# Optimization experiments

Hardware: AMD Instinct MI355X
Metric: run time of the kernel (lower is better)

The kernel has to match this reference:

```python
import jax, jax.numpy as jnp
import numpy as np

BSZ, DIM, SEQ_A, SEQ_B = 16, 768, 1024, 1024


def setup_inputs() -> dict:
    key = jax.random.key(0)
    kA, kB, kU = jax.random.split(key, 3)
    input_A = jax.random.normal(kA, (BSZ, DIM, SEQ_A), dtype=jnp.float32)
    input_B = jax.random.normal(kB, (BSZ, DIM, SEQ_B), dtype=jnp.float32)
    intput_msk = jnp.zeros((BSZ, SEQ_A, SEQ_B), dtype=jnp.float32)  # 0 = on, -inf = off
    U = jax.random.normal(kU, (DIM, DIM), dtype=jnp.float32)
    return {"input_A": input_A, "input_B": input_B, "intput_msk": intput_msk, "U": U}


def reference(input_A, input_B, intput_msk, U):
    # align[b,s,t] = tanh( A[b,:,s]^T U B[b,:,t] )  -> (bsz, seq_A, seq_B)
    align = jnp.einsum("bds,de,bet->bst", input_A, U, input_B)
    align = jnp.tanh(align) + intput_msk
    # per-token scores: max over the other modality's sequence, then softmax
    score_A = jax.nn.softmax(jnp.max(align, axis=2), axis=-1)  # (bsz, seq_A)
    score_B = jax.nn.softmax(jnp.max(align, axis=1), axis=-1)  # (bsz, seq_B)
    output_A = jnp.einsum("bds,bs->bd", input_A, score_A)  # (bsz, dim_A)
    output_B = jnp.einsum("bdt,bt->bd", input_B, score_B)  # (bsz, dim_B)
    return (output_A, output_B)
```

## Files before the change

### kernel.cpp

```cpp
#include <hip/hip_runtime.h>
#include <math.h>

#define BSZ  16
#define DIM  768
#define SEQA 1024
#define SEQB 1024

typedef float f32x4 __attribute__((ext_vector_type(4)));
typedef long long llong;

__device__ inline void gload_lds16(const void* g, void* l) {
    __builtin_amdgcn_global_load_lds(
        (const __attribute__((address_space(1))) void*)g,
        (__attribute__((address_space(3))) void*)l, 16, 0, 0);
}

__device__ inline unsigned enc_key(float f) {
    unsigned u = __float_as_uint(f);
    return (u & 0x80000000u) ? ~u : (u | 0x80000000u);
}
__device__ inline float dec_key(unsigned k) {
    return (k & 0x80000000u) ? __uint_as_float(k ^ 0x80000000u) : __uint_as_float(~k);
}

__device__ inline unsigned pk4_fp8(float a, float b, float c, float d) {
    int v = 0;
    v = __builtin_amdgcn_cvt_pk_fp8_f32(a, b, v, false);
    v = __builtin_amdgcn_cvt_pk_fp8_f32(c, d, v, true);
    return (unsigned)v;
}
__device__ inline unsigned char f2fp8(float a) {
    return (unsigned char)(__builtin_amdgcn_cvt_pk_fp8_f32(a, a, 0, false) & 0xFF);
}

__device__ inline float fast_tanh(float x) {
    float ax = fabsf(x);
    float u = __expf(-2.0f * ax);
    float th = __fdividef(1.0f - u, 1.0f + u);
    return copysignf(th, x);
}

__global__ __launch_bounds__(256) void t_cast_AB(const float* __restrict__ A,
                                                 const float* __restrict__ B,
                                                 unsigned char* __restrict__ At,
                                                 unsigned char* __restrict__ Bt) {
    __shared__ float tl[64][68];
    const int z = blockIdx.z;
    const float* X = (z < BSZ) ? A : B;
    unsigned char* Y = (z < BSZ) ? At : Bt;
    const int b = z & 15;
    const int d0 = blockIdx.y * 64;
    const int s0 = blockIdx.x * 64;
    const int tid = threadIdx.x;
    const int rr = tid >> 4, c4 = tid & 15;
    const float* Xb = X + ((size_t)b * DIM + d0) * SEQA + s0;
#pragma unroll
    for (int i = 0; i < 4; i++) {
        int row = i * 16 + rr;
        float4 v = *(const float4*)&Xb[(size_t)row * SEQA + c4 * 4];
        *(float4*)&tl[row][c4 * 4] = v;
    }
    __syncthreads();
    unsigned char* Yb = Y + ((size_t)b * SEQA + s0) * DIM + d0;
    const int m = tid & 15, sl = tid >> 4;
#pragma unroll
    for (int i = 0; i < 4; i++) {
        int s = sl + 16 * i;
        unsigned v = pk4_fp8(tl[4 * m + 0][s], tl[4 * m + 1][s], tl[4 * m + 2][s], tl[4 * m + 3][s]);
        *(unsigned*)&Yb[(size_t)s * DIM + 4 * m] = v;
    }
}

__global__ __launch_bounds__(256) void t_cast_U(const float* __restrict__ U,
                                                unsigned char* __restrict__ Ut,
                                                unsigned* __restrict__ keyA,
                                                unsigned* __restrict__ keyB) {
    __shared__ float tl[64][68];
    const int d0 = blockIdx.y * 64;
    const int e0 = blockIdx.x * 64;
    const int tid = threadIdx.x;
    const int bid = blockIdx.y * gridDim.x + blockIdx.x;
    if (bid < 64) {
        int i = bid * 256 + tid;
        keyA[i] = 0u;
        keyB[i] = 0u;
    }
    const int rr = tid >> 4, c4 = tid & 15;
#pragma unroll
    for (int i = 0; i < 4; i++) {
        int row = i * 16 + rr;
        float4 v = *(const float4*)&U[(size_t)(d0 + row) * DIM + e0 + c4 * 4];
        *(float4*)&tl[row][c4 * 4] = v;
    }
    __syncthreads();
    const int m = tid & 15, sl = tid >> 4;
#pragma unroll
    for (int i = 0; i < 4; i++) {
        int e = sl + 16 * i;
        unsigned v = pk4_fp8(tl[4 * m + 0][e], tl[4 * m + 1][e], tl[4 * m + 2][e], tl[4 * m + 3][e]);
        *(unsigned*)&Ut[(size_t)(e0 + e) * DIM + d0 + 4 * m] = v;
    }
}

__device__ inline void stage_tile(const unsigned char* __restrict__ src, int row0,
                                  int kbyte0, unsigned char* lds, int wid, int lane) {
    const int r8 = lane >> 3;
    const int g  = lane & 7;
    const int gg = g ^ (r8 & 7);
#pragma unroll
    for (int t = 0; t < 4; ++t) {
        int row = row0 + wid * 32 + t * 8 + r8;
        gload_lds16(src + (size_t)row * DIM + kbyte0 + gg * 16,
                    lds + (wid * 32 + t * 8) * 128 + lane * 16);
    }
}

__device__ inline llong frag_read(const unsigned char* lds, int rowbase, int l15,
                                  int quad, int h) {
    int gg = 2 * h + (quad >> 1);
    int off = (rowbase + l15) * 128 + ((gg ^ (l15 & 7)) << 4) + (quad & 1) * 8;
    return *(const llong*)(lds + off);
}

__global__ __launch_bounds__(256, 3) void k1_ua(const unsigned char* __restrict__ At,
                                                const unsigned char* __restrict__ Ut,
                                                unsigned char* __restrict__ Ct) {
    __shared__ __align__(16) unsigned char As[128 * 128];
    __shared__ __align__(16) unsigned char Us[128 * 128];
    const int b  = blockIdx.z;
    const int s0 = blockIdx.x * 128;
    const int e0 = blockIdx.y * 128;
    const int tid = threadIdx.x;
    const int lane = tid & 63;
    const int wid = tid >> 6;
    const int wr = wid >> 1, wc = wid & 1;
    const int quad = lane >> 4, l15 = lane & 15;

    const unsigned char* Atb = At + (size_t)b * SEQA * DIM;
    f32x4 acc[4][4] = {};

    for (int d0 = 0; d0 < DIM; d0 += 128) {
        stage_tile(Atb + (size_t)s0 * DIM, 0, d0, As, wid, lane);
        stage_tile(Ut + (size_t)e0 * DIM, 0, d0, Us, wid, lane);
        __syncthreads();
#pragma unroll
        for (int h = 0; h < 4; ++h) {
            llong av[4], bv[4];
#pragma unroll
            for (int i = 0; i < 4; ++i) av[i] = frag_read(As, wr * 64 + 16 * i, l15, quad, h);
#pragma unroll
            for (int j = 0; j < 4; ++j) bv[j] = frag_read(Us, wc * 64 + 16 * j, l15, quad, h);
#pragma unroll
            for (int i = 0; i < 4; ++i)
#pragma unroll
                for (int j = 0; j < 4; ++j)
                    acc[i][j] = __builtin_amdgcn_mfma_f32_16x16x32_fp8_fp8(av[i], bv[j], acc[i][j], 0, 0, 0);
        }
        __syncthreads();
    }
    unsigned char* Cb = Ct + (size_t)b * SEQA * DIM;
#pragma unroll
    for (int i = 0; i < 4; ++i)
#pragma unroll
        for (int j = 0; j < 4; ++j) {
            int e_g = e0 + wc * 64 + 16 * j + l15;
#pragma unroll
            for (int r = 0; r < 4; ++r) {
                int s_g = s0 + wr * 64 + 16 * i + quad * 4 + r;
                Cb[(size_t)s_g * DIM + e_g] = f2fp8(acc[i][j][r]);
            }
        }
}

__global__ __launch_bounds__(256, 4) void k2_align(const unsigned char* __restrict__ Ct,
                                                   const unsigned char* __restrict__ Bt,
                                                   const float* __restrict__ msk,
                                                   unsigned* __restrict__ keyA,
                                                   unsigned* __restrict__ keyB) {
    __shared__ __align__(16) unsigned char Cs[128 * 128];
    __shared__ __align__(16) unsigned char Bs[128 * 128];
    const int b  = blockIdx.z;
    const int t0 = blockIdx.x * 128;
    const int s0 = blockIdx.y * 128;
    const int tid = threadIdx.x;
    const int lane = tid & 63;
    const int wid = tid >> 6;
    const int wr = wid >> 1, wc = wid & 1;
    const int quad = lane >> 4, l15 = lane & 15;

    f32x4 acc[4][4] = {};

    for (int e0 = 0; e0 < DIM; e0 += 128) {
        stage_tile(Ct + (size_t)(b * SEQA + s0) * DIM, 0, e0, Cs, wid, lane);
        stage_tile(Bt + (size_t)(b * SEQB + t0) * DIM, 0, e0, Bs, wid, lane);
        __syncthreads();
#pragma unroll
        for (int h = 0; h < 4; ++h) {
            llong av[4], bv[4];
#pragma unroll
            for (int i = 0; i < 4; ++i) av[i] = frag_read(Bs, wr * 64 + 16 * i, l15, quad, h);
#pragma unroll
            for (int j = 0; j < 4; ++j) bv[j] = frag_read(Cs, wc * 64 + 16 * j, l15, quad, h);
#pragma unroll
            for (int i = 0; i < 4; ++i)
#pragma unroll
                for (int j = 0; j < 4; ++j)
                    acc[i][j] = __builtin_amdgcn_mfma_f32_16x16x32_fp8_fp8(av[i], bv[j], acc[i][j], 0, 0, 0);
        }
        __syncthreads();
    }

    const float* Mb = msk + (size_t)b * SEQA * SEQB;
#pragma unroll
    for (int j = 0; j < 4; ++j) {
        int s_g = s0 + wc * 64 + 16 * j + l15;
#pragma unroll
        for (int i = 0; i < 4; ++i) {
            int t_g = t0 + wr * 64 + 16 * i + quad * 4;
            float4 mvv = *(const float4*)&Mb[(size_t)s_g * SEQB + t_g];
            acc[i][j][0] = fast_tanh(acc[i][j][0]) + mvv.x;
            acc[i][j][1] = fast_tanh(acc[i][j][1]) + mvv.y;
            acc[i][j][2] = fast_tanh(acc[i][j][2]) + mvv.z;
            acc[i][j][3] = fast_tanh(acc[i][j][3]) + mvv.w;
        }
    }
#pragma unroll
    for (int j = 0; j < 4; ++j) {
        float m = -INFINITY;
#pragma unroll
        for (int i = 0; i < 4; ++i)
#pragma unroll
            for (int r = 0; r < 4; ++r) m = fmaxf(m, acc[i][j][r]);
        m = fmaxf(m, __shfl_xor(m, 16));
        m = fmaxf(m, __shfl_xor(m, 32));
        if (quad == 0)
            atomicMax(&keyA[b * SEQA + s0 + wc * 64 + 16 * j + l15], enc_key(m));
    }
#pragma unroll
    for (int i = 0; i < 4; ++i)
#pragma unroll
        for (int r = 0; r < 4; ++r) {
            float m = fmaxf(fmaxf(acc[i][0][r], acc[i][1][r]), fmaxf(acc[i][2][r], acc[i][3][r]));
            m = fmaxf(m, __shfl_xor(m, 1));
            m = fmaxf(m, __shfl_xor(m, 2));
            m = fmaxf(m, __shfl_xor(m, 4));
            m = fmaxf(m, __shfl_xor(m, 8));
            if (l15 == 0)
                atomicMax(&keyB[b * SEQB + t0 + wr * 64 + 16 * i + quad * 4 + r], enc_key(m));
        }
}

__global__ __launch_bounds__(256) void k3_softmax(const unsigned* __restrict__ keyA,
                                                  const unsigned* __restrict__ keyB,
                                                  float* __restrict__ scoreA,
                                                  float* __restrict__ scoreB) {
    const int b = blockIdx.x;
    const bool isA = (blockIdx.y == 0);
    const unsigned* keys = isA ? (keyA + b * SEQA) : (keyB + b * SEQB);
    float* score = isA ? (scoreA + b * SEQA) : (scoreB + b * SEQB);
    __shared__ float sh[4];
    const int tid = threadIdx.x;
    float m[4];
    float mx = -INFINITY;
#pragma unroll
    for (int k = 0; k < 4; k++) {
        m[k] = dec_key(keys[tid + 256 * k]);
        mx = fmaxf(mx, m[k]);
    }
#pragma unroll
    for (int o = 32; o > 0; o >>= 1) mx = fmaxf(mx, __shfl_down(mx, o, 64));
    if ((tid & 63) == 0) sh[tid >> 6] = mx;
    __syncthreads();
    mx = fmaxf(fmaxf(sh[0], sh[1]), fmaxf(sh[2], sh[3]));
    __syncthreads();
    float e[4];
    float sum = 0.f;
#pragma unroll
    for (int k = 0; k < 4; k++) { e[k] = expf(m[k] - mx); sum += e[k]; }
#pragma unroll
    for (int o = 32; o > 0; o >>= 1) sum += __shfl_down(sum, o, 64);
    if ((tid & 63) == 0) sh[tid >> 6] = sum;
    __syncthreads();
    sum = sh[0] + sh[1] + sh[2] + sh[3];
    float inv = 1.0f / sum;
#pragma unroll
    for (int k = 0; k < 4; k++) score[tid + 256 * k] = e[k] * inv;
}

__global__ __launch_bounds__(256) void k4_out(const float* __restrict__ A,
                                              const float* __restrict__ B,
                                              const float* __restrict__ scoreA,
                                              const float* __restrict__ scoreB,
                                              float* __restrict__ out) {
    const int which = blockIdx.y;
    const int row = blockIdx.x * 4 + (threadIdx.x >> 6);
    const int lane = threadIdx.x & 63;
    const float* X = which ? B : A;
    const float* S = which ? scoreB : scoreA;
    const int b = row / DIM;
    const float4* xr = (const float4*)(X + (size_t)row * SEQA);
    const float4* sr = (const float4*)(S + (size_t)b * SEQA);
    float acc = 0.f;
#pragma unroll
    for (int q = lane; q < SEQA / 4; q += 64) {
        float4 x = xr[q];
        float4 s = sr[q];
        acc += x.x * s.x + x.y * s.y + x.z * s.z + x.w * s.w;
    }
#pragma unroll
    for (int o = 32; o > 0; o >>= 1) acc += __shfl_down(acc, o, 64);
    if (lane == 0) out[which * (BSZ * DIM) + row] = acc;
}

extern "C" void kernel_launch(void* const* d_in, const int* in_sizes, int n_in,
                              void* d_out, int out_size, void* d_ws, size_t ws_size,
                              hipStream_t stream) {
    const float* A   = (const float*)d_in[0];
    const float* B   = (const float*)d_in[1];
    const float* msk = (const float*)d_in[2];
    const float* U   = (const float*)d_in[3];
    float* out = (float*)d_out;

    char* ws = (char*)d_ws;
    unsigned char* At = (unsigned char*)ws;
    unsigned char* Bt = (unsigned char*)(ws + 12582912);
    unsigned char* Ct = (unsigned char*)(ws + 25165824);
    unsigned char* Ut = (unsigned char*)(ws + 37748736);
    unsigned* keyA   = (unsigned*)(ws + 38338560);
    unsigned* keyB   = (unsigned*)(ws + 38404096);
    float*    scoreA = (float*)   (ws + 38469632);
    float*    scoreB = (float*)   (ws + 38535168);

    t_cast_U<<<dim3(DIM / 64, DIM / 64, 1), 256, 0, stream>>>(U, Ut, keyA, keyB);
    t_cast_AB<<<dim3(SEQA / 64, DIM / 64, 2 * BSZ), 256, 0, stream>>>(A, B, At, Bt);
    k1_ua<<<dim3(SEQA / 128, DIM / 128, BSZ), 256, 0, stream>>>(At, Ut, Ct);
    k2_align<<<dim3(SEQB / 128, SEQA / 128, BSZ), 256, 0, stream>>>(Ct, Bt, msk, keyA, keyB);
    k3_softmax<<<dim3(BSZ, 2), 256, 0, stream>>>(keyA, keyB, scoreA, scoreB);
    k4_out<<<dim3(BSZ * DIM / 4, 2), 256, 0, stream>>>(A, B, scoreA, scoreB, out);
}
```

Measured before the change: 237.3 us.

## Enlarge align-kernel tiles to 256x256 with double-buffered LDS prefetch pipeline

The align GEMM kernel now uses 512-thread blocks computing 256x256 output tiles, so each wave holds an 8x4 grid of MFMA accumulators. The K loop double-buffers LDS: the next K-slab is loaded while MFMAs run on the current one, with explicit vmcnt waits, barriers and raised wave priority around the MFMA bursts. The aim is to cut global traffic per FLOP and hide load latency behind compute. The cost is one block per CU with 128KB of LDS and more register pressure, and the grid shrinks to 256 blocks.

```diff
diff --git a/kernel.cpp b/kernel.cpp
--- a/kernel.cpp
+++ b/kernel.cpp
@@ -122,6 +122,8 @@
     return *(const llong*)(lds + off);
 }
 
+#define TB (256 * 128)
+
 __global__ __launch_bounds__(256, 3) void k1_ua(const unsigned char* __restrict__ At,
                                                 const unsigned char* __restrict__ Ut,
                                                 unsigned char* __restrict__ Ct) {
@@ -172,63 +174,98 @@
         }
 }
 
-__global__ __launch_bounds__(256, 4) void k2_align(const unsigned char* __restrict__ Ct,
+__global__ __launch_bounds__(512, 1) void k2_align(const unsigned char* __restrict__ Ct,
                                                    const unsigned char* __restrict__ Bt,
                                                    const float* __restrict__ msk,
                                                    unsigned* __restrict__ keyA,
                                                    unsigned* __restrict__ keyB) {
-    __shared__ __align__(16) unsigned char Cs[128 * 128];
-    __shared__ __align__(16) unsigned char Bs[128 * 128];
+    __shared__ __align__(16) unsigned char Bs[2 * TB];
+    __shared__ __align__(16) unsigned char Cs[2 * TB];
     const int b  = blockIdx.z;
-    const int t0 = blockIdx.x * 128;
-    const int s0 = blockIdx.y * 128;
+    const int t0 = blockIdx.x * 256;
+    const int s0 = blockIdx.y * 256;
     const int tid = threadIdx.x;
     const int lane = tid & 63;
     const int wid = tid >> 6;
-    const int wr = wid >> 1, wc = wid & 1;
+    const int wr = wid >> 2, wc = wid & 3;
     const int quad = lane >> 4, l15 = lane & 15;
 
-    f32x4 acc[4][4] = {};
-
-    for (int e0 = 0; e0 < DIM; e0 += 128) {
-        stage_tile(Ct + (size_t)(b * SEQA + s0) * DIM, 0, e0, Cs, wid, lane);
-        stage_tile(Bt + (size_t)(b * SEQB + t0) * DIM, 0, e0, Bs, wid, lane);
-        __syncthreads();
-#pragma unroll
-        for (int h = 0; h < 4; ++h) {
-            llong av[4], bv[4];
-#pragma unroll
-            for (int i = 0; i < 4; ++i) av[i] = frag_read(Bs, wr * 64 + 16 * i, l15, quad, h);
-#pragma unroll
-            for (int j = 0; j < 4; ++j) bv[j] = frag_read(Cs, wc * 64 + 16 * j, l15, quad, h);
-#pragma unroll
-            for (int i = 0; i < 4; ++i)
+    const unsigned char* Btb = Bt + ((size_t)b * SEQB + t0) * DIM;
+    const unsigned char* Ctb = Ct + ((size_t)b * SEQA + s0) * DIM;
+
+    f32x4 acc[8][4] = {};
+
+    stage_tile(Btb, 0, 0, Bs, wid, lane);
+    stage_tile(Ctb, 0, 0, Cs, wid, lane);
+    stage_tile(Btb, 0, 128, Bs + TB, wid, lane);
+    stage_tile(Ctb, 0, 128, Cs + TB, wid, lane);
+    asm volatile("s_waitcnt vmcnt(8)" ::: "memory");
+    __builtin_amdgcn_s_barrier();
+
+#pragma unroll 1
+    for (int kt = 0; kt < 6; ++kt) {
+        const unsigned char* MS_c = Bs + (kt & 1) * TB;
+        const unsigned char* NS_c = Cs + (kt & 1) * TB;
+        llong av[8], bv[4];
+#pragma unroll
+        for (int p = 0; p < 3; ++p) {
+#pragma unroll
+            for (int i = 0; i < 8; ++i) av[i] = frag_read(MS_c, wr * 128 + 16 * i, l15, quad, p);
+#pragma unroll
+            for (int j = 0; j < 4; ++j) bv[j] = frag_read(NS_c, wc * 64 + 16 * j, l15, quad, p);
+            __builtin_amdgcn_s_barrier();
+            asm volatile("s_waitcnt lgkmcnt(0)" ::: "memory");
+            __builtin_amdgcn_sched_barrier(0);
+            __builtin_amdgcn_s_setprio(1);
+#pragma unroll
+            for (int i = 0; i < 8; ++i)
 #pragma unroll
                 for (int j = 0; j < 4; ++j)
                     acc[i][j] = __builtin_amdgcn_mfma_f32_16x16x32_fp8_fp8(av[i], bv[j], acc[i][j], 0, 0, 0);
-        }
-        __syncthreads();
+            __builtin_amdgcn_s_setprio(0);
+            __builtin_amdgcn_s_barrier();
+        }
+#pragma unroll
+        for (int i = 0; i < 8; ++i) av[i] = frag_read(MS_c, wr * 128 + 16 * i, l15, quad, 3);
+#pragma unroll
+        for (int j = 0; j < 4; ++j) bv[j] = frag_read(NS_c, wc * 64 + 16 * j, l15, quad, 3);
+        asm volatile("s_waitcnt lgkmcnt(0)" ::: "memory");
+        __builtin_amdgcn_sched_barrier(0);
+        __builtin_amdgcn_s_barrier();
+        if (kt < 4) {
+            stage_tile(Btb, 0, (kt + 2) * 128, Bs + (kt & 1) * TB, wid, lane);
+            stage_tile(Ctb, 0, (kt + 2) * 128, Cs + (kt & 1) * TB, wid, lane);
+        }
+        __builtin_amdgcn_s_setprio(1);
+#pragma unroll
+        for (int i = 0; i < 8; ++i)
+#pragma unroll
+            for (int j = 0; j < 4; ++j)
+                acc[i][j] = __builtin_amdgcn_mfma_f32_16x16x32_fp8_fp8(av[i], bv[j], acc[i][j], 0, 0, 0);
+        __builtin_amdgcn_s_setprio(0);
+        if (kt < 4)       { asm volatile("s_waitcnt vmcnt(8)" ::: "memory"); }
+        else if (kt == 4) { asm volatile("s_waitcnt vmcnt(0)" ::: "memory"); }
+        __builtin_amdgcn_s_barrier();
     }
 
     const float* Mb = msk + (size_t)b * SEQA * SEQB;
 #pragma unroll
-    for (int j = 0; j < 4; ++j) {
-        int s_g = s0 + wc * 64 + 16 * j + l15;
-#pragma unroll
-        for (int i = 0; i < 4; ++i) {
-            int t_g = t0 + wr * 64 + 16 * i + quad * 4;
+    for (int i = 0; i < 8; ++i)
+#pragma unroll
+        for (int j = 0; j < 4; ++j) {
+            int s_g = s0 + wc * 64 + 16 * j + l15;
+            int t_g = t0 + wr * 128 + 16 * i + quad * 4;
             float4 mvv = *(const float4*)&Mb[(size_t)s_g * SEQB + t_g];
             acc[i][j][0] = fast_tanh(acc[i][j][0]) + mvv.x;
             acc[i][j][1] = fast_tanh(acc[i][j][1]) + mvv.y;
             acc[i][j][2] = fast_tanh(acc[i][j][2]) + mvv.z;
             acc[i][j][3] = fast_tanh(acc[i][j][3]) + mvv.w;
         }
-    }
 #pragma unroll
     for (int j = 0; j < 4; ++j) {
         float m = -INFINITY;
 #pragma unroll
-        for (int i = 0; i < 4; ++i)
+        for (int i = 0; i < 8; ++i)
 #pragma unroll
             for (int r = 0; r < 4; ++r) m = fmaxf(m, acc[i][j][r]);
         m = fmaxf(m, __shfl_xor(m, 16));
@@ -237,7 +274,7 @@
             atomicMax(&keyA[b * SEQA + s0 + wc * 64 + 16 * j + l15], enc_key(m));
     }
 #pragma unroll
-    for (int i = 0; i < 4; ++i)
+    for (int i = 0; i < 8; ++i)
 #pragma unroll
         for (int r = 0; r < 4; ++r) {
             float m = fmaxf(fmaxf(acc[i][0][r], acc[i][1][r]), fmaxf(acc[i][2][r], acc[i][3][r]));
@@ -246,7 +283,7 @@
             m = fmaxf(m, __shfl_xor(m, 4));
             m = fmaxf(m, __shfl_xor(m, 8));
             if (l15 == 0)
-                atomicMax(&keyB[b * SEQB + t0 + wr * 64 + 16 * i + quad * 4 + r], enc_key(m));
+                atomicMax(&keyB[b * SEQB + t0 + wr * 128 + 16 * i + quad * 4 + r], enc_key(m));
         }
 }
 
@@ -334,7 +371,7 @@
     t_cast_U<<<dim3(DIM / 64, DIM / 64, 1), 256, 0, stream>>>(U, Ut, keyA, keyB);
     t_cast_AB<<<dim3(SEQA / 64, DIM / 64, 2 * BSZ), 256, 0, stream>>>(A, B, At, Bt);
     k1_ua<<<dim3(SEQA / 128, DIM / 128, BSZ), 256, 0, stream>>>(At, Ut, Ct);
-    k2_align<<<dim3(SEQB / 128, SEQA / 128, BSZ), 256, 0, stream>>>(Ct, Bt, msk, keyA, keyB);
+    k2_align<<<dim3(SEQB / 256, SEQA / 256, BSZ), 512, 0, stream>>>(Ct, Bt, msk, keyA, keyB);
     k3_softmax<<<dim3(BSZ, 2), 256, 0, stream>>>(keyA, keyB, scoreA, scoreB);
     k4_out<<<dim3(BSZ * DIM / 4, 2), 256, 0, stream>>>(A, B, scoreA, scoreB, out);
 }
```

Measured after the change: 258.0 us. 8.7% more time.
